# Kernel tuning notes

Measured on AMD Instinct MI355X. Metric: run time of the kernel, lower is better.

The kernel has to match this reference:

```python
import jax, jax.numpy as jnp
import numpy as np

EMB = 128  # emb_dim (D)
HID = 2 * EMB  # MLPKernel hidden width (2D, since kernel input is concat[Phi_A, Phi_B])


def setup_inputs() -> dict:
    key = jax.random.key(0)
    ks = jax.random.split(key, 8)
    B, N, D = 2, 512, EMB
    s1 = 1.0 / np.sqrt(2 * D)
    s2 = 1.0 / np.sqrt(HID)
    return {
        "Phi_A": jax.random.normal(ks[0], (B, N, D), jnp.float32),
        "Phi_B": jax.random.normal(ks[1], (B, N, D), jnp.float32),
        # MLPKernel params: Linear(2D->2D) -> ReLU -> Linear(2D->2D) -> ReLU -> Linear(2D->1)
        "W1": jax.random.normal(ks[2], (2 * D, HID), jnp.float32) * s1,
        "b1": jnp.zeros((HID,), jnp.float32),
        "W2": jax.random.normal(ks[3], (HID, HID), jnp.float32) * s2,
        "b2": jnp.zeros((HID,), jnp.float32),
        "W3": jax.random.normal(ks[4], (HID, 1), jnp.float32) * s2,
        "b3": jnp.zeros((1,), jnp.float32),
    }


def reference(Phi_A, Phi_B, W1, b1, W2, b2, W3, b3):
    # Faithful to: kernel(cat[Phi_A_r, Phi_B_r]) over all N*N pairs -> dro [B,N,N].
    # First linear on concat == split-weight matmuls + broadcast add (same math,
    # avoids materializing the [B,N,N,2D] repeated tensor).
    D = Phi_A.shape[-1]
    hA = jnp.einsum("bnd,dh->bnh", Phi_A, W1[:D])   # [B,N,H]
    hB = jnp.einsum("bmd,dh->bmh", Phi_B, W1[D:])   # [B,M,H]
    h = jax.nn.relu(hA[:, :, None, :] + hB[:, None, :, :] + b1)  # [B,N,M,H]
    h = jax.nn.relu(jnp.einsum("bnmh,hk->bnmk", h, W2) + b2)      # [B,N,M,H]
    dro = (jnp.einsum("bnmh,hk->bnmk", h, W3) + b3)[..., 0]       # [B,N,M]
    return dro
```

## Files before the change

kernel.cpp:

```cpp
#include <hip/hip_runtime.h>
#include <hip/hip_bf16.h>

#define BB 2
#define NN 512
#define DD 128
#define HH 256

typedef __attribute__((ext_vector_type(4))) float  f32x4;
typedef __attribute__((ext_vector_type(8))) short  s16x8;
typedef __attribute__((ext_vector_type(4))) int    i32x4;

__device__ __forceinline__ float bf16u(short u) {
  return __int_as_float(((int)(unsigned short)u) << 16);
}
template <int CTRL>
__device__ __forceinline__ float dpp_add(float x) {
  int s = __builtin_amdgcn_update_dpp(0, __float_as_int(x), CTRL, 0xF, 0xF, true);
  return x + __int_as_float(s);
}

#define S1_ROWS 8
__global__ __launch_bounds__(256) void stage1(
    const float* __restrict__ PhiA, const float* __restrict__ PhiB,
    const float* __restrict__ W1,  const float* __restrict__ b1,
    __hip_bfloat16* __restrict__ hA, __hip_bfloat16* __restrict__ hB) {
  __shared__ float phis[S1_ROWS * DD];
  const int side = blockIdx.x & 1;
  const int row0 = (blockIdx.x >> 1) * S1_ROWS;
  const float* Phi = side ? PhiB : PhiA;
  const float* W   = W1 + side * DD * HH;
  ((f32x4*)phis)[threadIdx.x] =
      ((const f32x4*)(Phi + (size_t)row0 * DD))[threadIdx.x];
  __syncthreads();
  const int h = threadIdx.x;
  float acc[S1_ROWS];
#pragma unroll
  for (int i = 0; i < S1_ROWS; i++) acc[i] = 0.f;
  for (int d0 = 0; d0 < DD; d0 += 4) {
    const float w0 = W[(d0 + 0) * HH + h];
    const float w1 = W[(d0 + 1) * HH + h];
    const float w2 = W[(d0 + 2) * HH + h];
    const float w3 = W[(d0 + 3) * HH + h];
#pragma unroll
    for (int i = 0; i < S1_ROWS; i++) {
      f32x4 ph = *(const f32x4*)&phis[i * DD + d0];
      acc[i] = fmaf(ph.x, w0, acc[i]);
      acc[i] = fmaf(ph.y, w1, acc[i]);
      acc[i] = fmaf(ph.z, w2, acc[i]);
      acc[i] = fmaf(ph.w, w3, acc[i]);
    }
  }
  const float bias = side ? 0.f : b1[h];
  __hip_bfloat16* o = (side ? hB : hA) + (size_t)row0 * HH + h;
#pragma unroll
  for (int i = 0; i < S1_ROWS; i++) o[i * HH] = __float2bfloat16(acc[i] + bias);
}

__global__ __launch_bounds__(256) void prep_w2(
    const float* __restrict__ W2, __hip_bfloat16* __restrict__ W2t) {
  const int col = blockIdx.x;
  const int k   = threadIdx.x;
  W2t[col * HH + k] = __float2bfloat16(W2[k * HH + col]);
}

#define GRID_MAIN 512

__global__ __launch_bounds__(256, 2) void pairmlp(
    const __hip_bfloat16* __restrict__ hA, const __hip_bfloat16* __restrict__ hB,
    const __hip_bfloat16* __restrict__ W2t, const float* __restrict__ b2,
    const float* __restrict__ W3, const float* __restrict__ b3,
    float* __restrict__ out) {
  __shared__ __align__(16) short h1[2][32 * 256];

  const int tid  = threadIdx.x;
  const int lane = tid & 63;
  const int w    = tid >> 6;
  const int g    = lane >> 4;
  const int lr   = lane & 15;
  const int bid  = blockIdx.x;
  const int bb    = bid >> 8;
  const int m0    = (bid & 31) * 16;
  const int nbase = (bid & 255) >> 5;

  s16x8 breg[8][4];
#pragma unroll
  for (int ks = 0; ks < 8; ks++)
#pragma unroll
    for (int ct = 0; ct < 4; ct++) {
      const int col = w * 64 + ct * 16 + lr;
      breg[ks][ct] = *reinterpret_cast<const s16x8*>(&W2t[col * HH + ks * 32 + g * 8]);
    }
  float b2v[4], w3v[4];
#pragma unroll
  for (int ct = 0; ct < 4; ct++) {
    const int col = w * 64 + ct * 16 + lr;
    b2v[ct] = b2[col];
    w3v[ct] = W3[col];
  }
  const float b3q = b3[0] * 0.25f;

  const int p = tid >> 3;
  const int c = tid & 7;

  s16x8 hbr[4];
  {
    const __hip_bfloat16* hBp =
        hB + ((size_t)(bb * NN + m0 + (p & 15))) * HH + c * 32;
#pragma unroll
    for (int q = 0; q < 4; q++)
      hbr[q] = *reinterpret_cast<const s16x8*>(hBp + q * 8);
  }
  const __hip_bfloat16* hAbase =
      hA + ((size_t)(bb * NN + (p >> 4))) * HH + c * 32;

  auto loadA = [&](int n0, s16x8* av) {
    const __hip_bfloat16* hAp = hAbase + (size_t)n0 * HH;
#pragma unroll
    for (int q = 0; q < 4; q++)
      av[q] = *reinterpret_cast<const s16x8*>(hAp + q * 8);
  };
  auto build = [&](const s16x8* av, int buf) {
#pragma unroll
    for (int q = 0; q < 4; q++) {
      int pk[4];
#pragma unroll
      for (int jj = 0; jj < 4; jj++) {
        float r0 = fmaxf(bf16u(av[q][2 * jj])     + bf16u(hbr[q][2 * jj]),     0.f);
        float r1 = fmaxf(bf16u(av[q][2 * jj + 1]) + bf16u(hbr[q][2 * jj + 1]), 0.f);
        union { __hip_bfloat162 hh; int ii; } u;
        u.hh = __float22bfloat162_rn(make_float2(r0, r1));
        pk[jj] = u.ii;
      }
      i32x4 pv = {pk[0], pk[1], pk[2], pk[3]};
      const int addr = (p * 512 + c * 64 + q * 16) ^ ((p & 7) << 4);
      *reinterpret_cast<i32x4*>(reinterpret_cast<char*>(h1[buf]) + addr) = pv;
    }
  };

  {
    s16x8 av[4];
    loadA(2 * nbase, av);
    build(av, 0);
  }

  for (int k = 0; k < 32; k++) {
    const int cur = k & 1;
    const int n0  = 2 * nbase + 16 * k;
    __syncthreads();

    s16x8 av[4];
    if (k < 31) loadA(n0 + 16, av);

    f32x4 acc[2][4];
#pragma unroll
    for (int rt = 0; rt < 2; rt++)
#pragma unroll
      for (int ct = 0; ct < 4; ct++) acc[rt][ct] = (f32x4){0.f, 0.f, 0.f, 0.f};
#pragma unroll
    for (int ks = 0; ks < 8; ks++) {
      s16x8 afrag[2];
#pragma unroll
      for (int rt = 0; rt < 2; rt++) {
        const int row  = rt * 16 + lr;
        const int addr = (row * 512 + ks * 64 + g * 16) ^ ((row & 7) << 4);
        afrag[rt] = *reinterpret_cast<const s16x8*>(
            reinterpret_cast<const char*>(h1[cur]) + addr);
      }
#pragma unroll
      for (int rt = 0; rt < 2; rt++)
#pragma unroll
        for (int ct = 0; ct < 4; ct++)
          acc[rt][ct] = __builtin_amdgcn_mfma_f32_16x16x32_bf16(
              afrag[rt], breg[ks][ct], acc[rt][ct], 0, 0, 0);
    }

    if (k < 31) build(av, cur ^ 1);

    float part[2][4];
#pragma unroll
    for (int rt = 0; rt < 2; rt++)
#pragma unroll
      for (int r = 0; r < 4; r++) {
        float s = 0.f;
#pragma unroll
        for (int ct = 0; ct < 4; ct++)
          s += fmaxf(acc[rt][ct][r] + b2v[ct], 0.f) * w3v[ct];
        s = dpp_add<0xB1>(s);
        s = dpp_add<0x4E>(s);
        s = dpp_add<0x141>(s);
        s = dpp_add<0x140>(s);
        part[rt][r] = s;
      }
    if (lr == 0) {
#pragma unroll
      for (int rt = 0; rt < 2; rt++)
#pragma unroll
        for (int r = 0; r < 4; r++)
          atomicAdd(&out[((size_t)(bb * NN + n0 + rt)) * NN + m0 + g * 4 + r],
                    part[rt][r] + b3q);
    }
  }
}

extern "C" void kernel_launch(void* const* d_in, const int* in_sizes, int n_in,
                              void* d_out, int out_size, void* d_ws, size_t ws_size,
                              hipStream_t stream) {
  const float* PhiA = (const float*)d_in[0];
  const float* PhiB = (const float*)d_in[1];
  const float* W1   = (const float*)d_in[2];
  const float* b1   = (const float*)d_in[3];
  const float* W2   = (const float*)d_in[4];
  const float* b2   = (const float*)d_in[5];
  const float* W3   = (const float*)d_in[6];
  const float* b3   = (const float*)d_in[7];
  float* out = (float*)d_out;

  char* ws = (char*)d_ws;
  __hip_bfloat16* hA  = (__hip_bfloat16*)ws;
  __hip_bfloat16* hB  = (__hip_bfloat16*)(ws + (512u << 10));
  __hip_bfloat16* W2t = (__hip_bfloat16*)(ws + (1024u << 10));

  hipMemsetAsync(d_out, 0, (size_t)out_size * sizeof(float), stream);
  hipLaunchKernelGGL(stage1, dim3(2 * (BB * NN) / S1_ROWS), dim3(256), 0, stream,
                     PhiA, PhiB, W1, b1, hA, hB);
  hipLaunchKernelGGL(prep_w2, dim3(HH), dim3(256), 0, stream, W2, W2t);
  hipLaunchKernelGGL(pairmlp, dim3(GRID_MAIN), dim3(256), 0, stream,
                     hA, hB, W2t, b2, W3, b3, out);
}
```

Baseline: 166.4 us.

## Stream W2 fragments from cache, double occupancy, reduce via LDS instead of atomics

Stops keeping the full W2 B-fragments resident in registers (128 VGPRs) and loads them per k-step from global/L1, which lets launch bounds rise to 4 blocks per SIMD group and the grid double to 1024 blocks with 16 iterations each. Cross-wave output reduction moves from global atomicAdd to an LDS buffer summed by 32 threads with a plain store, deferred one iteration so it overlaps the next MMA pass. This also removes the output memset. The trade-off is extra global/cache traffic for W2 on every iteration in exchange for higher occupancy and no atomics.

```diff
diff --git a/kernel.cpp b/kernel.cpp
--- a/kernel.cpp
+++ b/kernel.cpp
@@ -63,14 +63,16 @@
   W2t[col * HH + k] = __float2bfloat16(W2[k * HH + col]);
 }
 
-#define GRID_MAIN 512
-
-__global__ __launch_bounds__(256, 2) void pairmlp(
+#define GRID_MAIN 1024
+#define KITERS 16
+
+__global__ __launch_bounds__(256, 4) void pairmlp(
     const __hip_bfloat16* __restrict__ hA, const __hip_bfloat16* __restrict__ hB,
     const __hip_bfloat16* __restrict__ W2t, const float* __restrict__ b2,
     const float* __restrict__ W3, const float* __restrict__ b3,
     float* __restrict__ out) {
   __shared__ __align__(16) short h1[2][32 * 256];
+  __shared__ float red[2][4][32];
 
   const int tid  = threadIdx.x;
   const int lane = tid & 63;
@@ -78,18 +80,10 @@
   const int g    = lane >> 4;
   const int lr   = lane & 15;
   const int bid  = blockIdx.x;
-  const int bb    = bid >> 8;
-  const int m0    = (bid & 31) * 16;
-  const int nbase = (bid & 255) >> 5;
-
-  s16x8 breg[8][4];
-#pragma unroll
-  for (int ks = 0; ks < 8; ks++)
-#pragma unroll
-    for (int ct = 0; ct < 4; ct++) {
-      const int col = w * 64 + ct * 16 + lr;
-      breg[ks][ct] = *reinterpret_cast<const s16x8*>(&W2t[col * HH + ks * 32 + g * 8]);
-    }
+  const int bb    = bid >> 9;
+  const int m0    = ((bid >> 4) & 31) * 16;
+  const int nbase = bid & 15;
+
   float b2v[4], w3v[4];
 #pragma unroll
   for (int ct = 0; ct < 4; ct++) {
@@ -97,7 +91,8 @@
     b2v[ct] = b2[col];
     w3v[ct] = W3[col];
   }
-  const float b3q = b3[0] * 0.25f;
+  const float b3v = b3[0];
+  const __hip_bfloat16* wb = W2t + (size_t)(w * 64 + lr) * HH + g * 8;
 
   const int p = tid >> 3;
   const int c = tid & 7;
@@ -143,13 +138,21 @@
     build(av, 0);
   }
 
-  for (int k = 0; k < 32; k++) {
+  for (int k = 0; k < KITERS; k++) {
     const int cur = k & 1;
-    const int n0  = 2 * nbase + 16 * k;
+    const int n0  = 2 * (nbase + 16 * k);
     __syncthreads();
 
     s16x8 av[4];
-    if (k < 31) loadA(n0 + 16, av);
+    if (k < KITERS - 1) loadA(n0 + 32, av);
+
+    if (k > 0 && tid < 32) {
+      const int pb = cur ^ 1;
+      const float v = red[pb][0][tid] + red[pb][1][tid] + red[pb][2][tid] +
+                      red[pb][3][tid] + b3v;
+      const int n = (n0 - 32) + (tid >> 4);
+      out[((size_t)(bb * NN + n)) * NN + m0 + (tid & 15)] = v;
+    }
 
     f32x4 acc[2][4];
 #pragma unroll
@@ -158,6 +161,10 @@
       for (int ct = 0; ct < 4; ct++) acc[rt][ct] = (f32x4){0.f, 0.f, 0.f, 0.f};
 #pragma unroll
     for (int ks = 0; ks < 8; ks++) {
+      s16x8 bfrag[4];
+#pragma unroll
+      for (int ct = 0; ct < 4; ct++)
+        bfrag[ct] = *reinterpret_cast<const s16x8*>(wb + ct * (16 * HH) + ks * 32);
       s16x8 afrag[2];
 #pragma unroll
       for (int rt = 0; rt < 2; rt++) {
@@ -171,10 +178,10 @@
 #pragma unroll
         for (int ct = 0; ct < 4; ct++)
           acc[rt][ct] = __builtin_amdgcn_mfma_f32_16x16x32_bf16(
-              afrag[rt], breg[ks][ct], acc[rt][ct], 0, 0, 0);
-    }
-
-    if (k < 31) build(av, cur ^ 1);
+              afrag[rt], bfrag[ct], acc[rt][ct], 0, 0, 0);
+    }
+
+    if (k < KITERS - 1) build(av, cur ^ 1);
 
     float part[2][4];
 #pragma unroll
@@ -196,9 +203,17 @@
       for (int rt = 0; rt < 2; rt++)
 #pragma unroll
         for (int r = 0; r < 4; r++)
-          atomicAdd(&out[((size_t)(bb * NN + n0 + rt)) * NN + m0 + g * 4 + r],
-                    part[rt][r] + b3q);
-    }
+          red[cur][w][rt * 16 + g * 4 + r] = part[rt][r];
+    }
+  }
+
+  __syncthreads();
+  if (tid < 32) {
+    const int pb = (KITERS - 1) & 1;
+    const float v = red[pb][0][tid] + red[pb][1][tid] + red[pb][2][tid] +
+                    red[pb][3][tid] + b3v;
+    const int n = 2 * (nbase + 16 * (KITERS - 1)) + (tid >> 4);
+    out[((size_t)(bb * NN + n)) * NN + m0 + (tid & 15)] = v;
   }
 }
 
@@ -220,7 +235,6 @@
   __hip_bfloat16* hB  = (__hip_bfloat16*)(ws + (512u << 10));
   __hip_bfloat16* W2t = (__hip_bfloat16*)(ws + (1024u << 10));
 
-  hipMemsetAsync(d_out, 0, (size_t)out_size * sizeof(float), stream);
   hipLaunchKernelGGL(stage1, dim3(2 * (BB * NN) / S1_ROWS), dim3(256), 0, stream,
                      PhiA, PhiB, W1, b1, hA, hB);
   hipLaunchKernelGGL(prep_w2, dim3(HH), dim3(256), 0, stream, W2, W2t);
```

After: 486.3 us. 192% more time.
